# Optimization experiments

Measured on AMD Instinct MI355X. Metric: run time of the kernel, lower is better.

Reference implementation:

```python
import jax, jax.numpy as jnp
import numpy as np

N_NODES = 100000
N_EDGES = 3200000
D_FEAT = 64


def setup_inputs() -> dict:
    key = jax.random.key(0)
    k_x, k_r, k_c, k_v = jax.random.split(key, 4)
    x = jax.random.normal(k_x, (N_NODES, D_FEAT), dtype=jnp.float32)
    edge_row = jax.random.randint(k_r, (N_EDGES,), 0, N_NODES, dtype=jnp.int64)
    edge_col = jax.random.randint(k_c, (N_EDGES,), 0, N_NODES, dtype=jnp.int64)
    # positive values mimicking symmetric-normalized adjacency weights
    edge_val = jax.random.uniform(k_v, (N_EDGES,), dtype=jnp.float32)
    t = jnp.zeros((1,), dtype=jnp.float32)  # ODE time, unused by this linear GCN step
    return {"t": t, "x": x, "edge_row": edge_row, "edge_col": edge_col, "edge_val": edge_val}


def reference(t, x, edge_row, edge_col, edge_val):
    # out = A_sparse @ x, COO SpMM as gather -> scale -> segment-sum scatter
    # gathered: [n_edges, d]
    gathered = edge_val[:, None] * x[edge_col]
    out = jax.ops.segment_sum(gathered, edge_row, num_segments=N_NODES)
    return out
```

## Files before the change

### kernel.cpp

```cpp
#include <hip/hip_runtime.h>
#include <hip/hip_bf16.h>
#include <hip/hip_fp16.h>

#define D 64
#define RB 128
#define NB_MAX 1024
#define NBLK1 512
#define P1CAP 6272
#define CAP 5120

typedef unsigned long long ull;
typedef unsigned short u16;

__device__ __forceinline__ ull pack_rec(float v, int r, int c) {
    return ((ull)__float_as_uint(v) << 32) |
           (ull)(((unsigned)(r & (RB - 1)) << 17) | (unsigned)c);
}

__global__ __launch_bounds__(256) void spmm_atomic_kernel(
    const float* __restrict__ x,
    const int*   __restrict__ edge_row,
    const int*   __restrict__ edge_col,
    const float* __restrict__ edge_val,
    float*       __restrict__ out,
    int n_edges)
{
    const int gtid = blockIdx.x * blockDim.x + threadIdx.x;
    const int wave = gtid >> 6;
    const int lane = threadIdx.x & 63;
    if (wave >= n_edges) return;
    const int   r = edge_row[wave];
    const int   c = edge_col[wave];
    const float v = edge_val[wave];
    atomicAdd(&out[(size_t)r * D + lane], v * x[(size_t)c * D + lane]);
}

__global__ __launch_bounds__(256) void p1_localsort_kernel(
    const int* __restrict__ rows, const int* __restrict__ cols,
    const float* __restrict__ vals,
    ull* __restrict__ staged, u16* __restrict__ counts, u16* __restrict__ startpos,
    int n_edges, int nb, int chunk)
{
    __shared__ ull stage[P1CAP];
    __shared__ int cnt[NB_MAX];
    __shared__ int s[256];
    const int t = threadIdx.x, blk = blockIdx.x;
    const int e0 = blk * chunk;
    const int e1 = min(e0 + chunk, n_edges);
    const int len = e1 - e0;

    for (int i = t; i < nb; i += 256) cnt[i] = 0;
    __syncthreads();

    for (int i = e0 + t * 4; i < e1; i += 1024) {
        if (i + 4 <= e1) {
            const int4 r4 = *(const int4*)(rows + i);
            atomicAdd(&cnt[r4.x >> 7], 1);
            atomicAdd(&cnt[r4.y >> 7], 1);
            atomicAdd(&cnt[r4.z >> 7], 1);
            atomicAdd(&cnt[r4.w >> 7], 1);
        } else {
            for (int k = i; k < e1; ++k) atomicAdd(&cnt[rows[k] >> 7], 1);
        }
    }
    __syncthreads();

    int pre[4], sum = 0;
    const int base = t * 4;
    #pragma unroll
    for (int k = 0; k < 4; ++k) {
        const int idx = base + k;
        const int c = (idx < nb) ? cnt[idx] : 0;
        if (idx < nb) counts[(size_t)idx * NBLK1 + blk] = (u16)c;
        pre[k] = sum; sum += c;
    }
    s[t] = sum;
    for (int off = 1; off < 256; off <<= 1) {
        __syncthreads();
        const int w = (t >= off) ? s[t - off] : 0;
        __syncthreads();
        s[t] += w;
    }
    const int texcl = s[t] - sum;
    __syncthreads();
    #pragma unroll
    for (int k = 0; k < 4; ++k) {
        const int idx = base + k;
        if (idx < nb) {
            const int e = texcl + pre[k];
            cnt[idx] = e;
            startpos[(size_t)idx * NBLK1 + blk] = (u16)e;
        }
    }
    __syncthreads();

    for (int i = e0 + t * 4; i < e1; i += 1024) {
        if (i + 4 <= e1) {
            const int4   r4 = *(const int4*)(rows + i);
            const int4   c4 = *(const int4*)(cols + i);
            const float4 v4 = *(const float4*)(vals + i);
            int p;
            p = atomicAdd(&cnt[r4.x >> 7], 1); stage[p] = pack_rec(v4.x, r4.x, c4.x);
            p = atomicAdd(&cnt[r4.y >> 7], 1); stage[p] = pack_rec(v4.y, r4.y, c4.y);
            p = atomicAdd(&cnt[r4.z >> 7], 1); stage[p] = pack_rec(v4.z, r4.z, c4.z);
            p = atomicAdd(&cnt[r4.w >> 7], 1); stage[p] = pack_rec(v4.w, r4.w, c4.w);
        } else {
            for (int k = i; k < e1; ++k) {
                const int p = atomicAdd(&cnt[rows[k] >> 7], 1);
                stage[p] = pack_rec(vals[k], rows[k], cols[k]);
            }
        }
    }
    __syncthreads();

    for (int i = t; i < len; i += 256)
        staged[(size_t)blk * chunk + i] = stage[i];
}

__global__ __launch_bounds__(256) void p2_binsum_kernel(
    const u16* __restrict__ counts, int* __restrict__ binsum, int nb)
{
    __shared__ int s[256];
    const int b = blockIdx.x, t = threadIdx.x;
    const int acc = (int)counts[(size_t)b * NBLK1 + t] +
                    (int)counts[(size_t)b * NBLK1 + t + 256];
    s[t] = acc;
    __syncthreads();
    for (int off = 128; off > 0; off >>= 1) {
        if (t < off) s[t] += s[t + off];
        __syncthreads();
    }
    if (t == 0) binsum[b] = s[0];
}

__global__ __launch_bounds__(1024) void p3_scanbins_kernel(
    const int* __restrict__ binsum, int* __restrict__ binbase,
    int* __restrict__ flags, int nb)
{
    __shared__ int s[1024];
    const int t = threadIdx.x;
    const int mine = (t < nb) ? binsum[t] : 0;
    s[t] = mine;
    for (int off = 1; off < 1024; off <<= 1) {
        __syncthreads();
        const int v = (t >= off) ? s[t - off] : 0;
        __syncthreads();
        s[t] += v;
    }
    if (t < nb) { binbase[t] = s[t] - mine; flags[t] = 0; }
    if (t == nb - 1) binbase[nb] = s[t];
}

__global__ __launch_bounds__(256) void p4_binsort_kernel(
    const ull* __restrict__ staged, const u16* __restrict__ counts,
    const u16* __restrict__ startpos, const int* __restrict__ binbase,
    ull* __restrict__ recs, int* __restrict__ offsets_row, int* __restrict__ flags,
    int nb, int n_nodes, int chunk)
{
    __shared__ ull stage[CAP];
    __shared__ int doff[NBLK1 + 1];
    __shared__ int srcs[NBLK1];
    __shared__ int cnt[1024];
    __shared__ int s[256];
    const int b = blockIdx.x, t = threadIdx.x;
    const int s0 = binbase[b];

    const int la = (int)counts[(size_t)b * NBLK1 + 2 * t];
    const int lb = (int)counts[(size_t)b * NBLK1 + 2 * t + 1];
    srcs[2 * t]     = (int)startpos[(size_t)b * NBLK1 + 2 * t];
    srcs[2 * t + 1] = (int)startpos[(size_t)b * NBLK1 + 2 * t + 1];
    const int mysum = la + lb;
    s[t] = mysum;
    for (int off = 1; off < 256; off <<= 1) {
        __syncthreads();
        const int w = (t >= off) ? s[t - off] : 0;
        __syncthreads();
        s[t] += w;
    }
    const int excl = s[t] - mysum;
    doff[2 * t] = excl;
    doff[2 * t + 1] = excl + la;
    if (t == 255) doff[NBLK1] = s[255];
    __syncthreads();
    const int len = doff[NBLK1];

    if (len > CAP) {
        if (t == 0) flags[b] = 1;
        for (int i = t; i < len; i += 256) {
            int lo = 0, hi = NBLK1 - 1;
            while (lo < hi) {
                const int mid = (lo + hi + 1) >> 1;
                if (doff[mid] <= i) lo = mid; else hi = mid - 1;
            }
            recs[s0 + i] = staged[(size_t)lo * chunk + srcs[lo] + (i - doff[lo])];
        }
        if (t == 0 && b * RB <= n_nodes) offsets_row[b * RB] = s0;
        return;
    }

    for (int i = t; i < 1024; i += 256) cnt[i] = 0;
    __syncthreads();

    for (int i = t; i < len; i += 256) {
        int lo = 0, hi = NBLK1 - 1;
        while (lo < hi) {
            const int mid = (lo + hi + 1) >> 1;
            if (doff[mid] <= i) lo = mid; else hi = mid - 1;
        }
        const ull rr = staged[(size_t)lo * chunk + srcs[lo] + (i - doff[lo])];
        stage[i] = rr;
        const int key = ((int)((rr >> 17) & (RB - 1)) << 3) |
                        (int)(((unsigned)rr & 0x1FFFF) >> 14);
        atomicAdd(&cnt[key], 1);
    }
    __syncthreads();

    int v[4], pre[4], sum = 0;
    const int base = t * 4;
    #pragma unroll
    for (int k = 0; k < 4; ++k) { v[k] = cnt[base + k]; pre[k] = sum; sum += v[k]; }
    s[t] = sum;
    for (int off = 1; off < 256; off <<= 1) {
        __syncthreads();
        const int w = (t >= off) ? s[t - off] : 0;
        __syncthreads();
        s[t] += w;
    }
    const int texcl = s[t] - sum;
    __syncthreads();
    #pragma unroll
    for (int k = 0; k < 4; ++k) cnt[base + k] = texcl + pre[k];
    __syncthreads();

    if (t <= RB) {
        const int r = b * RB + t;
        if (r <= n_nodes)
            offsets_row[r] = s0 + ((t == RB) ? len : cnt[t << 3]);
    }
    __syncthreads();

    for (int i = t; i < len; i += 256) {
        const ull rr = stage[i];
        const int key = ((int)((rr >> 17) & (RB - 1)) << 3) |
                        (int)(((unsigned)rr & 0x1FFFF) >> 14);
        const int p = atomicAdd(&cnt[key], 1);
        recs[s0 + p] = rr;
    }
}

__global__ void tohalf_kernel(const float* __restrict__ x,
                              __half2* __restrict__ xh2, int n4)
{
    for (int i = blockIdx.x * blockDim.x + threadIdx.x; i < n4;
         i += gridDim.x * blockDim.x) {
        const float4 v = ((const float4*)x)[i];
        xh2[2 * i + 0] = __floats2half2_rn(v.x, v.y);
        xh2[2 * i + 1] = __floats2half2_rn(v.z, v.w);
    }
}

__global__ __launch_bounds__(256, 8) void spmm_csr_half_kernel(
    const __half* __restrict__ xh,
    const int*   __restrict__ offsets_row,
    const int*   __restrict__ binbase,
    const ull*   __restrict__ recs,
    const int*   __restrict__ flags,
    float*       __restrict__ out,
    int n_nodes)
{
    const int row  = blockIdx.x * 4 + (threadIdx.x >> 6);
    const int lane = threadIdx.x & 63;
    if (row >= n_nodes) return;

    float acc = 0.f;
    const int b = row >> 7;

    if (__builtin_expect(flags[b], 0)) {
        const int s  = binbase[b];
        const int e  = binbase[b + 1];
        const int lr = row & (RB - 1);
        for (int j = s; j < e; ++j) {
            const ull rec = recs[j];
            if ((int)((rec >> 17) & (RB - 1)) == lr) {
                const int   c = (int)((unsigned)rec & 0x1FFFF);
                const float v = __uint_as_float((unsigned)(rec >> 32));
                acc += v * __half2float(xh[(size_t)c * D + lane]);
            }
        }
    } else {
        const int s = offsets_row[row];
        const int e = offsets_row[row + 1];
        int j = s;
        for (; j + 8 <= e; j += 8) {
            float vv[8];
            int   aa[8];
            #pragma unroll
            for (int k = 0; k < 8; ++k) {
                const ull rec = recs[j + k];
                vv[k] = __uint_as_float((unsigned)(rec >> 32));
                aa[k] = (int)((unsigned)rec & 0x1FFFF) * D + lane;
            }
            __half hv[8];
            #pragma unroll
            for (int k = 0; k < 8; ++k)
                hv[k] = xh[aa[k]];
            __builtin_amdgcn_sched_barrier(0);
            #pragma unroll
            for (int k = 0; k < 8; ++k)
                acc += vv[k] * __half2float(hv[k]);
        }
        for (; j < e; ++j) {
            const ull rec = recs[j];
            const float v = __uint_as_float((unsigned)(rec >> 32));
            const int   c = (int)((unsigned)rec & 0x1FFFF);
            acc += v * __half2float(xh[(size_t)c * D + lane]);
        }
    }
    out[(size_t)row * D + lane] = acc;
}

static inline size_t align16(size_t v) { return (v + 15) & ~(size_t)15; }

extern "C" void kernel_launch(void* const* d_in, const int* in_sizes, int n_in,
                              void* d_out, int out_size, void* d_ws, size_t ws_size,
                              hipStream_t stream)
{
    const float* x        = (const float*)d_in[1];
    const int*   edge_row = (const int*)d_in[2];
    const int*   edge_col = (const int*)d_in[3];
    const float* edge_val = (const float*)d_in[4];
    float*       out      = (float*)d_out;

    const int n_edges = in_sizes[2];
    const int n_nodes = out_size / D;
    const int nb      = (n_nodes + RB - 1) / RB;
    const int chunk   = (((n_edges + NBLK1 - 1) / NBLK1) + 3) & ~3;

    const size_t off_recs    = 0;
    const size_t off_staged  = align16(off_recs + (size_t)n_edges * 8);
    const size_t off_counts  = align16(off_staged + (size_t)NBLK1 * chunk * 8);
    const size_t off_start   = align16(off_counts + (size_t)nb * NBLK1 * 2);
    const size_t off_binsum  = align16(off_start + (size_t)nb * NBLK1 * 2);
    const size_t off_binbase = align16(off_binsum + (size_t)nb * 4);
    const size_t off_rowoffs = align16(off_binbase + (size_t)(nb + 1) * 4);
    const size_t off_flags   = align16(off_rowoffs + (size_t)(n_nodes + 1) * 4);
    const size_t ws_needed   = off_flags + (size_t)nb * 4;
    const size_t xh_bytes    = (size_t)n_nodes * D * 2;

    if (ws_size < ws_needed || nb > NB_MAX || n_nodes > (1 << 17) ||
        chunk > P1CAP || xh_bytes > (size_t)NBLK1 * chunk * 8) {
        hipMemsetAsync(out, 0, (size_t)out_size * sizeof(float), stream);
        const int n_blocks = (n_edges + 3) / 4;
        spmm_atomic_kernel<<<n_blocks, 256, 0, stream>>>(
            x, edge_row, edge_col, edge_val, out, n_edges);
        return;
    }

    char* ws = (char*)d_ws;
    ull*    recs        = (ull*)(ws + off_recs);
    ull*    staged      = (ull*)(ws + off_staged);
    u16*    counts      = (u16*)(ws + off_counts);
    u16*    startpos    = (u16*)(ws + off_start);
    int*    binsum      = (int*)(ws + off_binsum);
    int*    binbase     = (int*)(ws + off_binbase);
    int*    offsets_row = (int*)(ws + off_rowoffs);
    int*    flags       = (int*)(ws + off_flags);
    __half* xh          = (__half*)(ws + off_staged);

    p1_localsort_kernel<<<NBLK1, 256, 0, stream>>>(
        edge_row, edge_col, edge_val, staged, counts, startpos,
        n_edges, nb, chunk);
    p2_binsum_kernel<<<nb, 256, 0, stream>>>(counts, binsum, nb);
    p3_scanbins_kernel<<<1, 1024, 0, stream>>>(binsum, binbase, flags, nb);
    p4_binsort_kernel<<<nb, 256, 0, stream>>>(
        staged, counts, startpos, binbase, recs, offsets_row, flags,
        nb, n_nodes, chunk);
    const int n4 = (n_nodes * D) / 4;
    tohalf_kernel<<<2048, 256, 0, stream>>>(x, (__half2*)xh, n4);
    spmm_csr_half_kernel<<<(n_nodes + 3) / 4, 256, 0, stream>>>(
        xh, offsets_row, binbase, recs, flags, out, n_nodes);
}
```

Before: 277.7 us.

## Replace two-level bin sort with global counting sort and half2 SpMM

Drops the block-local staging sort, bin sums and per-bin LDS sort. In their place it runs a global histogram over (row, column-octant) keys with global atomics, a three-pass scan and an atomic-cursor scatter straight into CSR records. The SpMM kernel now reads half2 features, with each half-wave handling alternating edges, and combines the two halves with a shuffle. This removes the overflow fallback path and the staging memory traffic. In exchange it adds heavy global atomic contention in the histogram and scatter, a memset, and scattered 8-byte writes.

```diff
diff --git a/kernel.cpp b/kernel.cpp
--- a/kernel.cpp
+++ b/kernel.cpp
@@ -1,21 +1,9 @@
 #include <hip/hip_runtime.h>
-#include <hip/hip_bf16.h>
 #include <hip/hip_fp16.h>
 
 #define D 64
-#define RB 128
-#define NB_MAX 1024
-#define NBLK1 512
-#define P1CAP 6272
-#define CAP 5120
 
 typedef unsigned long long ull;
-typedef unsigned short u16;
-
-__device__ __forceinline__ ull pack_rec(float v, int r, int c) {
-    return ((ull)__float_as_uint(v) << 32) |
-           (ull)(((unsigned)(r & (RB - 1)) << 17) | (unsigned)c);
-}
 
 __global__ __launch_bounds__(256) void spmm_atomic_kernel(
     const float* __restrict__ x,
@@ -35,216 +23,125 @@
     atomicAdd(&out[(size_t)r * D + lane], v * x[(size_t)c * D + lane]);
 }
 
-__global__ __launch_bounds__(256) void p1_localsort_kernel(
+__global__ __launch_bounds__(256) void hist_kernel(
+    const int* __restrict__ rows, const int* __restrict__ cols,
+    int* __restrict__ hist, int n_edges)
+{
+    const int i = (blockIdx.x * 256 + threadIdx.x) * 4;
+    if (i + 4 <= n_edges) {
+        const int4 r = *(const int4*)(rows + i);
+        const int4 c = *(const int4*)(cols + i);
+        atomicAdd(&hist[(r.x << 3) | (c.x >> 14)], 1);
+        atomicAdd(&hist[(r.y << 3) | (c.y >> 14)], 1);
+        atomicAdd(&hist[(r.z << 3) | (c.z >> 14)], 1);
+        atomicAdd(&hist[(r.w << 3) | (c.w >> 14)], 1);
+    } else {
+        for (int k = i; k < n_edges; ++k)
+            atomicAdd(&hist[(rows[k] << 3) | (cols[k] >> 14)], 1);
+    }
+}
+
+__global__ __launch_bounds__(1024) void scan1_kernel(
+    const int* __restrict__ hist, int* __restrict__ keybase,
+    int* __restrict__ sums, int nkeys)
+{
+    __shared__ int s[1024];
+    const int t    = threadIdx.x;
+    const int base = blockIdx.x * 4096 + t * 4;
+    int4 v = make_int4(0, 0, 0, 0);
+    if (base + 4 <= nkeys) {
+        v = *(const int4*)(hist + base);
+    } else {
+        if (base + 0 < nkeys) v.x = hist[base + 0];
+        if (base + 1 < nkeys) v.y = hist[base + 1];
+        if (base + 2 < nkeys) v.z = hist[base + 2];
+        if (base + 3 < nkeys) v.w = hist[base + 3];
+    }
+    const int sum = v.x + v.y + v.z + v.w;
+    s[t] = sum;
+    for (int off = 1; off < 1024; off <<= 1) {
+        __syncthreads();
+        const int w = (t >= off) ? s[t - off] : 0;
+        __syncthreads();
+        s[t] += w;
+    }
+    const int excl = s[t] - sum;
+    if (t == 1023) sums[blockIdx.x] = s[t];
+    int4 o;
+    o.x = excl;
+    o.y = o.x + v.x;
+    o.z = o.y + v.y;
+    o.w = o.z + v.z;
+    if (base + 4 <= nkeys) {
+        *(int4*)(keybase + base) = o;
+    } else {
+        if (base + 0 < nkeys) keybase[base + 0] = o.x;
+        if (base + 1 < nkeys) keybase[base + 1] = o.y;
+        if (base + 2 < nkeys) keybase[base + 2] = o.z;
+        if (base + 3 < nkeys) keybase[base + 3] = o.w;
+    }
+}
+
+__global__ __launch_bounds__(256) void scan2_kernel(int* __restrict__ sums, int n)
+{
+    __shared__ int s[256];
+    const int t = threadIdx.x;
+    const int v = (t < n) ? sums[t] : 0;
+    s[t] = v;
+    for (int off = 1; off < 256; off <<= 1) {
+        __syncthreads();
+        const int w = (t >= off) ? s[t - off] : 0;
+        __syncthreads();
+        s[t] += w;
+    }
+    if (t < n) sums[t] = s[t] - v;
+}
+
+__global__ __launch_bounds__(256) void scan3_kernel(
+    int* __restrict__ keybase, int* __restrict__ cursor,
+    const int* __restrict__ sums, int nkeys, int n_edges)
+{
+    const int base = (blockIdx.x * 256 + threadIdx.x) * 4;
+    const int add  = sums[blockIdx.x >> 2];
+    if (base + 4 <= nkeys) {
+        int4 v = *(const int4*)(keybase + base);
+        v.x += add; v.y += add; v.z += add; v.w += add;
+        *(int4*)(keybase + base) = v;
+        *(int4*)(cursor + base)  = v;
+    } else {
+        for (int k = base; k < nkeys; ++k) {
+            const int v = keybase[k] + add;
+            keybase[k] = v;
+            cursor[k]  = v;
+        }
+    }
+    if (blockIdx.x == 0 && threadIdx.x == 0) keybase[nkeys] = n_edges;
+}
+
+__global__ __launch_bounds__(256) void scatter_kernel(
     const int* __restrict__ rows, const int* __restrict__ cols,
     const float* __restrict__ vals,
-    ull* __restrict__ staged, u16* __restrict__ counts, u16* __restrict__ startpos,
-    int n_edges, int nb, int chunk)
-{
-    __shared__ ull stage[P1CAP];
-    __shared__ int cnt[NB_MAX];
-    __shared__ int s[256];
-    const int t = threadIdx.x, blk = blockIdx.x;
-    const int e0 = blk * chunk;
-    const int e1 = min(e0 + chunk, n_edges);
-    const int len = e1 - e0;
-
-    for (int i = t; i < nb; i += 256) cnt[i] = 0;
-    __syncthreads();
-
-    for (int i = e0 + t * 4; i < e1; i += 1024) {
-        if (i + 4 <= e1) {
-            const int4 r4 = *(const int4*)(rows + i);
-            atomicAdd(&cnt[r4.x >> 7], 1);
-            atomicAdd(&cnt[r4.y >> 7], 1);
-            atomicAdd(&cnt[r4.z >> 7], 1);
-            atomicAdd(&cnt[r4.w >> 7], 1);
-        } else {
-            for (int k = i; k < e1; ++k) atomicAdd(&cnt[rows[k] >> 7], 1);
-        }
-    }
-    __syncthreads();
-
-    int pre[4], sum = 0;
-    const int base = t * 4;
-    #pragma unroll
-    for (int k = 0; k < 4; ++k) {
-        const int idx = base + k;
-        const int c = (idx < nb) ? cnt[idx] : 0;
-        if (idx < nb) counts[(size_t)idx * NBLK1 + blk] = (u16)c;
-        pre[k] = sum; sum += c;
-    }
-    s[t] = sum;
-    for (int off = 1; off < 256; off <<= 1) {
-        __syncthreads();
-        const int w = (t >= off) ? s[t - off] : 0;
-        __syncthreads();
-        s[t] += w;
-    }
-    const int texcl = s[t] - sum;
-    __syncthreads();
-    #pragma unroll
-    for (int k = 0; k < 4; ++k) {
-        const int idx = base + k;
-        if (idx < nb) {
-            const int e = texcl + pre[k];
-            cnt[idx] = e;
-            startpos[(size_t)idx * NBLK1 + blk] = (u16)e;
-        }
-    }
-    __syncthreads();
-
-    for (int i = e0 + t * 4; i < e1; i += 1024) {
-        if (i + 4 <= e1) {
-            const int4   r4 = *(const int4*)(rows + i);
-            const int4   c4 = *(const int4*)(cols + i);
-            const float4 v4 = *(const float4*)(vals + i);
-            int p;
-            p = atomicAdd(&cnt[r4.x >> 7], 1); stage[p] = pack_rec(v4.x, r4.x, c4.x);
-            p = atomicAdd(&cnt[r4.y >> 7], 1); stage[p] = pack_rec(v4.y, r4.y, c4.y);
-            p = atomicAdd(&cnt[r4.z >> 7], 1); stage[p] = pack_rec(v4.z, r4.z, c4.z);
-            p = atomicAdd(&cnt[r4.w >> 7], 1); stage[p] = pack_rec(v4.w, r4.w, c4.w);
-        } else {
-            for (int k = i; k < e1; ++k) {
-                const int p = atomicAdd(&cnt[rows[k] >> 7], 1);
-                stage[p] = pack_rec(vals[k], rows[k], cols[k]);
-            }
-        }
-    }
-    __syncthreads();
-
-    for (int i = t; i < len; i += 256)
-        staged[(size_t)blk * chunk + i] = stage[i];
-}
-
-__global__ __launch_bounds__(256) void p2_binsum_kernel(
-    const u16* __restrict__ counts, int* __restrict__ binsum, int nb)
-{
-    __shared__ int s[256];
-    const int b = blockIdx.x, t = threadIdx.x;
-    const int acc = (int)counts[(size_t)b * NBLK1 + t] +
-                    (int)counts[(size_t)b * NBLK1 + t + 256];
-    s[t] = acc;
-    __syncthreads();
-    for (int off = 128; off > 0; off >>= 1) {
-        if (t < off) s[t] += s[t + off];
-        __syncthreads();
-    }
-    if (t == 0) binsum[b] = s[0];
-}
-
-__global__ __launch_bounds__(1024) void p3_scanbins_kernel(
-    const int* __restrict__ binsum, int* __restrict__ binbase,
-    int* __restrict__ flags, int nb)
-{
-    __shared__ int s[1024];
-    const int t = threadIdx.x;
-    const int mine = (t < nb) ? binsum[t] : 0;
-    s[t] = mine;
-    for (int off = 1; off < 1024; off <<= 1) {
-        __syncthreads();
-        const int v = (t >= off) ? s[t - off] : 0;
-        __syncthreads();
-        s[t] += v;
-    }
-    if (t < nb) { binbase[t] = s[t] - mine; flags[t] = 0; }
-    if (t == nb - 1) binbase[nb] = s[t];
-}
-
-__global__ __launch_bounds__(256) void p4_binsort_kernel(
-    const ull* __restrict__ staged, const u16* __restrict__ counts,
-    const u16* __restrict__ startpos, const int* __restrict__ binbase,
-    ull* __restrict__ recs, int* __restrict__ offsets_row, int* __restrict__ flags,
-    int nb, int n_nodes, int chunk)
-{
-    __shared__ ull stage[CAP];
-    __shared__ int doff[NBLK1 + 1];
-    __shared__ int srcs[NBLK1];
-    __shared__ int cnt[1024];
-    __shared__ int s[256];
-    const int b = blockIdx.x, t = threadIdx.x;
-    const int s0 = binbase[b];
-
-    const int la = (int)counts[(size_t)b * NBLK1 + 2 * t];
-    const int lb = (int)counts[(size_t)b * NBLK1 + 2 * t + 1];
-    srcs[2 * t]     = (int)startpos[(size_t)b * NBLK1 + 2 * t];
-    srcs[2 * t + 1] = (int)startpos[(size_t)b * NBLK1 + 2 * t + 1];
-    const int mysum = la + lb;
-    s[t] = mysum;
-    for (int off = 1; off < 256; off <<= 1) {
-        __syncthreads();
-        const int w = (t >= off) ? s[t - off] : 0;
-        __syncthreads();
-        s[t] += w;
-    }
-    const int excl = s[t] - mysum;
-    doff[2 * t] = excl;
-    doff[2 * t + 1] = excl + la;
-    if (t == 255) doff[NBLK1] = s[255];
-    __syncthreads();
-    const int len = doff[NBLK1];
-
-    if (len > CAP) {
-        if (t == 0) flags[b] = 1;
-        for (int i = t; i < len; i += 256) {
-            int lo = 0, hi = NBLK1 - 1;
-            while (lo < hi) {
-                const int mid = (lo + hi + 1) >> 1;
-                if (doff[mid] <= i) lo = mid; else hi = mid - 1;
-            }
-            recs[s0 + i] = staged[(size_t)lo * chunk + srcs[lo] + (i - doff[lo])];
-        }
-        if (t == 0 && b * RB <= n_nodes) offsets_row[b * RB] = s0;
-        return;
-    }
-
-    for (int i = t; i < 1024; i += 256) cnt[i] = 0;
-    __syncthreads();
-
-    for (int i = t; i < len; i += 256) {
-        int lo = 0, hi = NBLK1 - 1;
-        while (lo < hi) {
-            const int mid = (lo + hi + 1) >> 1;
-            if (doff[mid] <= i) lo = mid; else hi = mid - 1;
-        }
-        const ull rr = staged[(size_t)lo * chunk + srcs[lo] + (i - doff[lo])];
-        stage[i] = rr;
-        const int key = ((int)((rr >> 17) & (RB - 1)) << 3) |
-                        (int)(((unsigned)rr & 0x1FFFF) >> 14);
-        atomicAdd(&cnt[key], 1);
-    }
-    __syncthreads();
-
-    int v[4], pre[4], sum = 0;
-    const int base = t * 4;
-    #pragma unroll
-    for (int k = 0; k < 4; ++k) { v[k] = cnt[base + k]; pre[k] = sum; sum += v[k]; }
-    s[t] = sum;
-    for (int off = 1; off < 256; off <<= 1) {
-        __syncthreads();
-        const int w = (t >= off) ? s[t - off] : 0;
-        __syncthreads();
-        s[t] += w;
-    }
-    const int texcl = s[t] - sum;
-    __syncthreads();
-    #pragma unroll
-    for (int k = 0; k < 4; ++k) cnt[base + k] = texcl + pre[k];
-    __syncthreads();
-
-    if (t <= RB) {
-        const int r = b * RB + t;
-        if (r <= n_nodes)
-            offsets_row[r] = s0 + ((t == RB) ? len : cnt[t << 3]);
-    }
-    __syncthreads();
-
-    for (int i = t; i < len; i += 256) {
-        const ull rr = stage[i];
-        const int key = ((int)((rr >> 17) & (RB - 1)) << 3) |
-                        (int)(((unsigned)rr & 0x1FFFF) >> 14);
-        const int p = atomicAdd(&cnt[key], 1);
-        recs[s0 + p] = rr;
+    int* __restrict__ cursor, ull* __restrict__ recs, int n_edges)
+{
+    const int i = (blockIdx.x * 256 + threadIdx.x) * 4;
+    if (i + 4 <= n_edges) {
+        const int4   r = *(const int4*)(rows + i);
+        const int4   c = *(const int4*)(cols + i);
+        const float4 v = *(const float4*)(vals + i);
+        int p;
+        p = atomicAdd(&cursor[(r.x << 3) | (c.x >> 14)], 1);
+        recs[p] = ((ull)__float_as_uint(v.x) << 32) | (unsigned)c.x;
+        p = atomicAdd(&cursor[(r.y << 3) | (c.y >> 14)], 1);
+        recs[p] = ((ull)__float_as_uint(v.y) << 32) | (unsigned)c.y;
+        p = atomicAdd(&cursor[(r.z << 3) | (c.z >> 14)], 1);
+        recs[p] = ((ull)__float_as_uint(v.z) << 32) | (unsigned)c.z;
+        p = atomicAdd(&cursor[(r.w << 3) | (c.w >> 14)], 1);
+        recs[p] = ((ull)__float_as_uint(v.w) << 32) | (unsigned)c.w;
+    } else {
+        for (int k = i; k < n_edges; ++k) {
+            const int p = atomicAdd(&cursor[(rows[k] << 3) | (cols[k] >> 14)], 1);
+            recs[p] = ((ull)__float_as_uint(vals[k]) << 32) | (unsigned)cols[k];
+        }
     }
 }
 
@@ -259,64 +156,72 @@
     }
 }
 
-__global__ __launch_bounds__(256, 8) void spmm_csr_half_kernel(
-    const __half* __restrict__ xh,
-    const int*   __restrict__ offsets_row,
-    const int*   __restrict__ binbase,
-    const ull*   __restrict__ recs,
-    const int*   __restrict__ flags,
-    float*       __restrict__ out,
+__global__ __launch_bounds__(256, 8) void spmm_csr_half2_kernel(
+    const __half2* __restrict__ xh2,
+    const int*     __restrict__ keybase,
+    const ull*     __restrict__ recs,
+    float*         __restrict__ out,
     int n_nodes)
 {
-    const int row  = blockIdx.x * 4 + (threadIdx.x >> 6);
+    const int row = blockIdx.x * 4 + (threadIdx.x >> 6);
+    if (row >= n_nodes) return;
     const int lane = threadIdx.x & 63;
-    if (row >= n_nodes) return;
-
-    float acc = 0.f;
-    const int b = row >> 7;
-
-    if (__builtin_expect(flags[b], 0)) {
-        const int s  = binbase[b];
-        const int e  = binbase[b + 1];
-        const int lr = row & (RB - 1);
-        for (int j = s; j < e; ++j) {
-            const ull rec = recs[j];
-            if ((int)((rec >> 17) & (RB - 1)) == lr) {
-                const int   c = (int)((unsigned)rec & 0x1FFFF);
-                const float v = __uint_as_float((unsigned)(rec >> 32));
-                acc += v * __half2float(xh[(size_t)c * D + lane]);
-            }
-        }
-    } else {
-        const int s = offsets_row[row];
-        const int e = offsets_row[row + 1];
-        int j = s;
-        for (; j + 8 <= e; j += 8) {
-            float vv[8];
-            int   aa[8];
-            #pragma unroll
-            for (int k = 0; k < 8; ++k) {
-                const ull rec = recs[j + k];
-                vv[k] = __uint_as_float((unsigned)(rec >> 32));
-                aa[k] = (int)((unsigned)rec & 0x1FFFF) * D + lane;
-            }
-            __half hv[8];
-            #pragma unroll
-            for (int k = 0; k < 8; ++k)
-                hv[k] = xh[aa[k]];
-            __builtin_amdgcn_sched_barrier(0);
-            #pragma unroll
-            for (int k = 0; k < 8; ++k)
-                acc += vv[k] * __half2float(hv[k]);
-        }
-        for (; j < e; ++j) {
-            const ull rec = recs[j];
-            const float v = __uint_as_float((unsigned)(rec >> 32));
-            const int   c = (int)((unsigned)rec & 0x1FFFF);
-            acc += v * __half2float(xh[(size_t)c * D + lane]);
-        }
-    }
-    out[(size_t)row * D + lane] = acc;
+    const int half = lane >> 5;
+    const int fl   = lane & 31;
+
+    const int s = keybase[row << 3];
+    const int e = keybase[(row << 3) + 8];
+    float accx = 0.f, accy = 0.f;
+
+    int j = s;
+    for (; j + 16 <= e; j += 16) {
+        float vv[8]; int aa[8];
+        #pragma unroll
+        for (int k = 0; k < 8; ++k) {
+            const ull rec = recs[j + 2 * k + half];
+            vv[k] = __uint_as_float((unsigned)(rec >> 32));
+            aa[k] = ((int)((unsigned)rec & 0x1FFFF) << 5) + fl;
+        }
+        __half2 hv[8];
+        #pragma unroll
+        for (int k = 0; k < 8; ++k) hv[k] = xh2[aa[k]];
+        __builtin_amdgcn_sched_barrier(0);
+        #pragma unroll
+        for (int k = 0; k < 8; ++k) {
+            const float2 xf = __half22float2(hv[k]);
+            accx = fmaf(vv[k], xf.x, accx);
+            accy = fmaf(vv[k], xf.y, accy);
+        }
+    }
+    if (j < e) {
+        const int safe = e - 1;
+        float vv[8]; int aa[8];
+        #pragma unroll
+        for (int k = 0; k < 8; ++k) {
+            const int  idx = j + 2 * k + half;
+            const bool ok  = idx < e;
+            const ull  rec = recs[ok ? idx : safe];
+            vv[k] = ok ? __uint_as_float((unsigned)(rec >> 32)) : 0.f;
+            aa[k] = ((int)((unsigned)rec & 0x1FFFF) << 5) + fl;
+        }
+        __half2 hv[8];
+        #pragma unroll
+        for (int k = 0; k < 8; ++k) hv[k] = xh2[aa[k]];
+        __builtin_amdgcn_sched_barrier(0);
+        #pragma unroll
+        for (int k = 0; k < 8; ++k) {
+            const float2 xf = __half22float2(hv[k]);
+            accx = fmaf(vv[k], xf.x, accx);
+            accy = fmaf(vv[k], xf.y, accy);
+        }
+    }
+
+    accx += __shfl_xor(accx, 32);
+    accy += __shfl_xor(accy, 32);
+    if (half == 0) {
+        float2 o; o.x = accx; o.y = accy;
+        ((float2*)out)[(size_t)row * 32 + fl] = o;
+    }
 }
 
 static inline size_t align16(size_t v) { return (v + 15) & ~(size_t)15; }
@@ -333,22 +238,18 @@
 
     const int n_edges = in_sizes[2];
     const int n_nodes = out_size / D;
-    const int nb      = (n_nodes + RB - 1) / RB;
-    const int chunk   = (((n_edges + NBLK1 - 1) / NBLK1) + 3) & ~3;
-
-    const size_t off_recs    = 0;
-    const size_t off_staged  = align16(off_recs + (size_t)n_edges * 8);
-    const size_t off_counts  = align16(off_staged + (size_t)NBLK1 * chunk * 8);
-    const size_t off_start   = align16(off_counts + (size_t)nb * NBLK1 * 2);
-    const size_t off_binsum  = align16(off_start + (size_t)nb * NBLK1 * 2);
-    const size_t off_binbase = align16(off_binsum + (size_t)nb * 4);
-    const size_t off_rowoffs = align16(off_binbase + (size_t)(nb + 1) * 4);
-    const size_t off_flags   = align16(off_rowoffs + (size_t)(n_nodes + 1) * 4);
-    const size_t ws_needed   = off_flags + (size_t)nb * 4;
-    const size_t xh_bytes    = (size_t)n_nodes * D * 2;
-
-    if (ws_size < ws_needed || nb > NB_MAX || n_nodes > (1 << 17) ||
-        chunk > P1CAP || xh_bytes > (size_t)NBLK1 * chunk * 8) {
+    const int nkeys   = n_nodes * 8;
+    const int nscan1  = (nkeys + 4095) >> 12;
+
+    const size_t off_recs = 0;
+    const size_t off_xh   = align16(off_recs + (size_t)n_edges * 8);
+    const size_t off_keyb = align16(off_xh + (size_t)n_nodes * D * 2);
+    const size_t off_cur  = align16(off_keyb + (size_t)(nkeys + 1) * 4);
+    const size_t off_hist = align16(off_cur + (size_t)nkeys * 4);
+    const size_t off_sums = align16(off_hist + (size_t)nkeys * 4);
+    const size_t ws_needed = off_sums + (size_t)nscan1 * 4;
+
+    if (ws_size < ws_needed || n_nodes > (1 << 17) || n_edges < 1 || nscan1 > 256) {
         hipMemsetAsync(out, 0, (size_t)out_size * sizeof(float), stream);
         const int n_blocks = (n_edges + 3) / 4;
         spmm_atomic_kernel<<<n_blocks, 256, 0, stream>>>(
@@ -356,27 +257,26 @@
         return;
     }
 
-    char* ws = (char*)d_ws;
-    ull*    recs        = (ull*)(ws + off_recs);
-    ull*    staged      = (ull*)(ws + off_staged);
-    u16*    counts      = (u16*)(ws + off_counts);
-    u16*    startpos    = (u16*)(ws + off_start);
-    int*    binsum      = (int*)(ws + off_binsum);
-    int*    binbase     = (int*)(ws + off_binbase);
-    int*    offsets_row = (int*)(ws + off_rowoffs);
-    int*    flags       = (int*)(ws + off_flags);
-    __half* xh          = (__half*)(ws + off_staged);
-
-    p1_localsort_kernel<<<NBLK1, 256, 0, stream>>>(
-        edge_row, edge_col, edge_val, staged, counts, startpos,
-        n_edges, nb, chunk);
-    p2_binsum_kernel<<<nb, 256, 0, stream>>>(counts, binsum, nb);
-    p3_scanbins_kernel<<<1, 1024, 0, stream>>>(binsum, binbase, flags, nb);
-    p4_binsort_kernel<<<nb, 256, 0, stream>>>(
-        staged, counts, startpos, binbase, recs, offsets_row, flags,
-        nb, n_nodes, chunk);
+    char*   ws      = (char*)d_ws;
+    ull*    recs    = (ull*)(ws + off_recs);
+    __half* xh      = (__half*)(ws + off_xh);
+    int*    keybase = (int*)(ws + off_keyb);
+    int*    cursor  = (int*)(ws + off_cur);
+    int*    hist    = (int*)(ws + off_hist);
+    int*    sums    = (int*)(ws + off_sums);
+
+    const int n_eblk = (n_edges + 1023) / 1024;
+
+    hipMemsetAsync(hist, 0, (size_t)nkeys * 4, stream);
+    hist_kernel<<<n_eblk, 256, 0, stream>>>(edge_row, edge_col, hist, n_edges);
+    scan1_kernel<<<nscan1, 1024, 0, stream>>>(hist, keybase, sums, nkeys);
+    scan2_kernel<<<1, 256, 0, stream>>>(sums, nscan1);
+    scan3_kernel<<<(nkeys + 1023) / 1024, 256, 0, stream>>>(
+        keybase, cursor, sums, nkeys, n_edges);
+    scatter_kernel<<<n_eblk, 256, 0, stream>>>(
+        edge_row, edge_col, edge_val, cursor, recs, n_edges);
     const int n4 = (n_nodes * D) / 4;
     tohalf_kernel<<<2048, 256, 0, stream>>>(x, (__half2*)xh, n4);
-    spmm_csr_half_kernel<<<(n_nodes + 3) / 4, 256, 0, stream>>>(
-        xh, offsets_row, binbase, recs, flags, out, n_nodes);
-}
+    spmm_csr_half2_kernel<<<(n_nodes + 3) / 4, 256, 0, stream>>>(
+        (const __half2*)xh, keybase, recs, out, n_nodes);
+}
```

After: 556.1 us. +100.3%, slower.
